# Kernel tuning notes

Hardware: AMD Instinct MI355X
Metric: run time of the kernel (lower is better)

The kernel has to match this reference:

```python
import jax, jax.numpy as jnp
import numpy as np

TOP_K = 2  # num_expert in the torch module


def setup_inputs() -> dict:
    key = jax.random.key(0)
    ks = jax.random.split(key, 8)
    B, C, H, W, E, Dh = 8, 512, 32, 32, 8, 1024
    inputs = jax.random.normal(ks[0], (B, C, H, W), dtype=jnp.float32)
    k = jax.random.uniform(ks[1], (B, 1, 1, 1), dtype=jnp.float32)
    # gate: global-avg-pool + Linear(C -> E)
    Wg = jax.random.normal(ks[2], (C, E), dtype=jnp.float32) / np.sqrt(C)
    bg = jnp.zeros((E,), dtype=jnp.float32)
    # experts: per-expert 2-layer channel MLP (1x1-conv style), modulated by k
    W1 = jax.random.normal(ks[3], (E, C, Dh), dtype=jnp.float32) / np.sqrt(C)
    b1 = jnp.zeros((E, Dh), dtype=jnp.float32)
    W2 = jax.random.normal(ks[4], (E, Dh, C), dtype=jnp.float32) / np.sqrt(Dh)
    b2 = jnp.zeros((E, C), dtype=jnp.float32)
    return {"inputs": inputs, "k": k, "Wg": Wg, "bg": bg,
            "W1": W1, "b1": b1, "W2": W2, "b2": b2}


def reference(inputs, k, Wg, bg, W1, b1, W2, b2):
    B = inputs.shape[0]
    # --- gate: softmax in fp32, cast back (matches F.softmax(dtype=torch.float)) ---
    logits = jnp.mean(inputs, axis=(2, 3)) @ Wg + bg            # [B, E]
    weights = jax.nn.softmax(logits.astype(jnp.float32), axis=1).astype(inputs.dtype)
    topk_w, topk_idx = jax.lax.top_k(weights, TOP_K)            # [B, K]
    # --- scatter top-k gate weights into dense [B, E] mask (training path) ---
    exp_w = jnp.zeros_like(weights).at[jnp.arange(B)[:, None], topk_idx].set(topk_w)
    # --- run ALL experts densely (training-mode math), masked combine ---
    h = jnp.einsum('bchw,ecd->bedhw', inputs, W1) + b1[None, :, :, None, None]
    h = jax.nn.gelu(h, approximate=False)                        # [B,E,Dh,H,W]
    y = jnp.einsum('bedhw,edc->bechw', h, W2) + b2[None, :, :, None, None]
    y = y * k[:, None]                                           # per-sample scalar mod
    out = inputs + jnp.einsum('bechw,be->bchw', y, exp_w)        # residual + weighted sum
    return out
```

## Files before the change

### kernel.cpp

```cpp
#include <hip/hip_runtime.h>
#include <hip/hip_bf16.h>
#include <math.h>


typedef __bf16 bf16_t;
typedef __attribute__((ext_vector_type(8))) __bf16 bf16x8;
typedef __attribute__((ext_vector_type(4))) __bf16 bf16x4;
typedef __attribute__((ext_vector_type(4))) float f32x4;

#define GLDS(g, l) __builtin_amdgcn_global_load_lds(                      \
    (const __attribute__((address_space(1))) void*)(const void*)(g),       \
    (__attribute__((address_space(3))) void*)(void*)(l), 16, 0, 0)

__device__ __forceinline__ float gelu_fast(float x) {
    float z = x * 0.70710678118654752f;
    float az = fabsf(z);
    float t = 1.0f / (1.0f + 0.3275911f * az);
    float p = ((((1.061405429f * t - 1.453152027f) * t + 1.421413741f) * t
                - 0.284496736f) * t + 0.254829592f) * t;
    float e = __expf(-az * az);
    float er = copysignf(1.0f - p * e, z);
    return 0.5f * x * (1.0f + er);
}

__global__ void transpose_cvt_all(const float* __restrict__ x, const float* __restrict__ W1,
                                  const float* __restrict__ W2, bf16_t* __restrict__ xT,
                                  bf16_t* __restrict__ W1t, bf16_t* __restrict__ W2t,
                                  float* __restrict__ msum) {
    int id = blockIdx.x;
    const float* src; bf16_t* dst; int R, Cols, csh; bool dm = false;
    if (id < 4096)      { src = x;  dst = xT;  R = 512;  Cols = 1024; csh = 5; dm = true; }
    else if (id < 8192) { id -= 4096; src = W1; dst = W1t; R = 512;  Cols = 1024; csh = 5; }
    else                { id -= 8192; src = W2; dst = W2t; R = 1024; Cols = 512; csh = 4; }
    const int bz = id >> 9, t = id & 511;
    const int c0 = (t & ((1 << csh) - 1)) * 32, r0 = (t >> csh) * 32;
    const float* s = src + (size_t)bz * R * Cols;
    bf16_t* d = dst + (size_t)bz * R * Cols;
    __shared__ float tile[32][33];
    const int tid = threadIdx.x;
    const int lr = tid >> 3, lc = (tid & 7) * 4;
    float4 v = *(const float4*)(s + (size_t)(r0 + lr) * Cols + c0 + lc);
    tile[lr][lc + 0] = v.x; tile[lr][lc + 1] = v.y;
    tile[lr][lc + 2] = v.z; tile[lr][lc + 3] = v.w;
    if (dm) {
        float ps = v.x + v.y + v.z + v.w;
        ps += __shfl_down(ps, 4, 8);
        ps += __shfl_down(ps, 2, 8);
        ps += __shfl_down(ps, 1, 8);
        if ((tid & 7) == 0) atomicAdd(&msum[bz * 512 + r0 + lr], ps);
    }
    __syncthreads();
    bf16x4 o = { (bf16_t)tile[lc + 0][lr], (bf16_t)tile[lc + 1][lr],
                 (bf16_t)tile[lc + 2][lr], (bf16_t)tile[lc + 3][lr] };
    *(bf16x4*)(d + (size_t)(c0 + lr) * R + r0 + lc) = o;
}

__global__ void gate_kernel(const float* __restrict__ msum, const float* __restrict__ Wg,
                            const float* __restrict__ bg, const float* __restrict__ kmod,
                            int* __restrict__ tidx, float* __restrict__ scale) {
    const int tid = threadIdx.x;
    const int b = tid >> 6, l = tid & 63;
    float a[8] = {0.f, 0.f, 0.f, 0.f, 0.f, 0.f, 0.f, 0.f};
    for (int c = l; c < 512; c += 64) {
        float m = msum[b * 512 + c];
        #pragma unroll
        for (int e = 0; e < 8; ++e) a[e] += m * Wg[c * 8 + e];
    }
    #pragma unroll
    for (int e = 0; e < 8; ++e)
        #pragma unroll
        for (int off = 32; off; off >>= 1) a[e] += __shfl_xor(a[e], off, 64);
    if (l == 0) {
        float lg[8], mx = -1e30f;
        #pragma unroll
        for (int e = 0; e < 8; ++e) { lg[e] = a[e] * (1.0f / 1024.0f) + bg[e]; mx = fmaxf(mx, lg[e]); }
        float sum = 0.f;
        #pragma unroll
        for (int e = 0; e < 8; ++e) { lg[e] = expf(lg[e] - mx); sum += lg[e]; }
        float inv = 1.0f / sum;
        float best = -1.f; int i0 = 0;
        for (int j = 0; j < 8; ++j) { float w = lg[j] * inv; if (w > best) { best = w; i0 = j; } }
        float best2 = -1.f; int i1 = 0;
        for (int j = 0; j < 8; ++j) { if (j == i0) continue; float w = lg[j] * inv; if (w > best2) { best2 = w; i1 = j; } }
        float kb = kmod[b];
        tidx[b * 2] = i0; tidx[b * 2 + 1] = i1;
        scale[b * 2] = best * kb; scale[b * 2 + 1] = best2 * kb;
    }
}

__global__ __launch_bounds__(256, 4) void gemm1_kernel(
    const bf16_t* __restrict__ W1t, const bf16_t* __restrict__ xT,
    const float* __restrict__ b1, const int* __restrict__ tidx,
    const float* __restrict__ scale, bf16_t* __restrict__ hT) {
    __shared__ bf16_t smem[16384];
    const int bid = blockIdx.x;
    const int pair = bid >> 6, rem = bid & 63;
    const int b = pair >> 1, slot = pair & 1;
    const int e = tidx[pair];
    const float s = scale[pair];
    const int d0 = (rem >> 3) * 128, n0 = (rem & 7) * 128;
    const int tid = threadIdx.x;
    const int lane = tid & 63, wave = tid >> 6;
    const int wm = (wave & 1) * 64, wn = (wave >> 1) * 64;
    const int lrow = lane & 15, quad = lane >> 4;

    const bf16_t* gA = W1t + (size_t)e * 524288 + (size_t)d0 * 512;
    const bf16_t* gB = xT + (size_t)b * 524288 + (size_t)n0 * 512;
    const int r0s = tid >> 2, kcs = (tid & 3) * 8;
    f32x4 acc[4][4];
    #pragma unroll
    for (int i = 0; i < 4; ++i)
        #pragma unroll
        for (int j = 0; j < 4; ++j) acc[i][j] = (f32x4){0.f, 0.f, 0.f, 0.f};

    GLDS(gA + r0s * 512 + kcs, smem + tid * 8);
    GLDS(gA + (64 + r0s) * 512 + kcs, smem + (256 + tid) * 8);
    GLDS(gB + r0s * 512 + kcs, smem + 8192 + tid * 8);
    GLDS(gB + (64 + r0s) * 512 + kcs, smem + 8192 + (256 + tid) * 8);
    __syncthreads();

    for (int it = 0; it < 16; ++it) {
        const int cur = it & 1;
        if (it < 15) {
            const int kn = (it + 1) * 32;
            bf16_t* dA = smem + (cur ^ 1) * 4096;
            bf16_t* dB = smem + 8192 + (cur ^ 1) * 4096;
            GLDS(gA + r0s * 512 + kn + kcs, dA + tid * 8);
            GLDS(gA + (64 + r0s) * 512 + kn + kcs, dA + (256 + tid) * 8);
            GLDS(gB + r0s * 512 + kn + kcs, dB + tid * 8);
            GLDS(gB + (64 + r0s) * 512 + kn + kcs, dB + (256 + tid) * 8);
        }
        const bf16_t* cA = smem + cur * 4096;
        const bf16_t* cB = smem + 8192 + cur * 4096;
        bf16x8 af[4], bfr[4];
        #pragma unroll
        for (int i = 0; i < 4; ++i) {
            af[i] = *(const bf16x8*)&cA[(wm + i * 16 + lrow) * 32 + quad * 8];
            bfr[i] = *(const bf16x8*)&cB[(wn + i * 16 + lrow) * 32 + quad * 8];
        }
        #pragma unroll
        for (int i = 0; i < 4; ++i)
            #pragma unroll
            for (int j = 0; j < 4; ++j)
                acc[i][j] = __builtin_amdgcn_mfma_f32_16x16x32_bf16(af[i], bfr[j], acc[i][j], 0, 0, 0);
        __syncthreads();
    }

    bf16_t* hTb = hT + (size_t)b * 2097152 + slot * 1024;
    float4 bb[4];
    #pragma unroll
    for (int i = 0; i < 4; ++i)
        bb[i] = *(const float4*)(b1 + e * 1024 + d0 + wm + i * 16 + quad * 4);

    for (int half = 0; half < 2; ++half) {
        if (wn == half * 64) {
            #pragma unroll
            for (int i = 0; i < 4; ++i)
                #pragma unroll
                for (int j = 0; j < 4; ++j) {
                    const int hw_l = j * 16 + lrow;
                    const int d_l = wm + i * 16 + quad * 4;
                    f32x4 a = acc[i][j];
                    bf16x4 o = { (bf16_t)(gelu_fast(a[0] + bb[i].x) * s),
                                 (bf16_t)(gelu_fast(a[1] + bb[i].y) * s),
                                 (bf16_t)(gelu_fast(a[2] + bb[i].z) * s),
                                 (bf16_t)(gelu_fast(a[3] + bb[i].w) * s) };
                    *(bf16x4*)&smem[hw_l * 136 + d_l] = o;
                }
        }
        __syncthreads();
        #pragma unroll
        for (int q = 0; q < 4; ++q) {
            const int cid = q * 256 + tid;
            const int row = cid >> 4, c16 = cid & 15;
            bf16x8 v = *(const bf16x8*)&smem[row * 136 + c16 * 8];
            *(bf16x8*)(hTb + (size_t)(n0 + half * 64 + row) * 2048 + d0 + c16 * 8) = v;
        }
        __syncthreads();
    }
}

__global__ __launch_bounds__(256, 5) void gemm2_kernel(
    const bf16_t* __restrict__ W2t, const bf16_t* __restrict__ hT,
    const float* __restrict__ b2, const int* __restrict__ tidx,
    const float* __restrict__ scale, const float* __restrict__ x,
    float* __restrict__ out) {
    __shared__ bf16_t smem[16384];
    const int bid = blockIdx.x;
    const int b = bid >> 7, rem = bid & 127;
    const int c0 = (rem >> 4) * 64, n0 = (rem & 15) * 64;
    const int e0 = tidx[b * 2], e1 = tidx[b * 2 + 1];
    const float s0 = scale[b * 2], s1 = scale[b * 2 + 1];
    const int tid = threadIdx.x;
    const int lane = tid & 63, wave = tid >> 6;
    const int wm = (wave & 1) * 32, wn = (wave >> 1) * 32;
    const int lrow = lane & 15, quad = lane >> 4;

    const bf16_t* hTb = hT + (size_t)b * 2097152 + (size_t)n0 * 2048;
    const bf16_t* A0 = W2t + (size_t)e0 * 524288 + (size_t)c0 * 1024;
    const bf16_t* A1 = W2t + (size_t)e1 * 524288 + (size_t)c0 * 1024;
    const int sr = tid >> 2, kcs = (tid & 3) * 8;

    f32x4 acc[2][2];
    #pragma unroll
    for (int i = 0; i < 2; ++i)
        #pragma unroll
        for (int j = 0; j < 2; ++j) acc[i][j] = (f32x4){0.f, 0.f, 0.f, 0.f};

    auto stage = [&](int st, int it) {
        const int k0 = it * 64;
        const bf16_t* gA = ((k0 < 1024) ? A0 : A1) + (size_t)sr * 1024 + (k0 & 1023);
        bf16_t* dA = smem + st * 4096;
        bf16_t* dB = smem + 8192 + st * 4096;
        GLDS(gA + kcs, dA + tid * 8);
        GLDS(gA + 32 + kcs, dA + 2048 + tid * 8);
        const bf16_t* gBp = hTb + (size_t)sr * 2048 + k0;
        GLDS(gBp + kcs, dB + tid * 8);
        GLDS(gBp + 32 + kcs, dB + 2048 + tid * 8);
    };

    stage(0, 0);
    __syncthreads();

    for (int it = 0; it < 32; ++it) {
        const int cur = it & 1;
        if (it < 31) stage(cur ^ 1, it + 1);
        const bf16_t* cA = smem + cur * 4096;
        const bf16_t* cB = smem + 8192 + cur * 4096;
        #pragma unroll
        for (int ks = 0; ks < 2; ++ks) {
            bf16x8 af[2], bfr[2];
            #pragma unroll
            for (int i = 0; i < 2; ++i) {
                af[i] = *(const bf16x8*)&cA[ks * 2048 + (wm + i * 16 + lrow) * 32 + quad * 8];
                bfr[i] = *(const bf16x8*)&cB[ks * 2048 + (wn + i * 16 + lrow) * 32 + quad * 8];
            }
            #pragma unroll
            for (int i = 0; i < 2; ++i)
                #pragma unroll
                for (int j = 0; j < 2; ++j)
                    acc[i][j] = __builtin_amdgcn_mfma_f32_16x16x32_bf16(af[i], bfr[j], acc[i][j], 0, 0, 0);
        }
        __syncthreads();
    }

    #pragma unroll
    for (int i = 0; i < 2; ++i) {
        const int c_l = c0 + wm + i * 16 + quad * 4;
        const float4 bA = *(const float4*)(b2 + e0 * 512 + c_l);
        const float4 bB = *(const float4*)(b2 + e1 * 512 + c_l);
        const float bias[4] = { s0 * bA.x + s1 * bB.x, s0 * bA.y + s1 * bB.y,
                                s0 * bA.z + s1 * bB.z, s0 * bA.w + s1 * bB.w };
        #pragma unroll
        for (int j = 0; j < 2; ++j) {
            const int hw = n0 + wn + j * 16 + lrow;
            #pragma unroll
            for (int r = 0; r < 4; ++r) {
                const size_t o = (size_t)(b * 512 + c_l + r) * 1024 + hw;
                out[o] = x[o] + acc[i][j][r] + bias[r];
            }
        }
    }
}

extern "C" void kernel_launch(void* const* d_in, const int* in_sizes, int n_in,
                              void* d_out, int out_size, void* d_ws, size_t ws_size,
                              hipStream_t stream) {
    const float* x    = (const float*)d_in[0];
    const float* kmod = (const float*)d_in[1];
    const float* Wg   = (const float*)d_in[2];
    const float* bg   = (const float*)d_in[3];
    const float* W1   = (const float*)d_in[4];
    const float* b1   = (const float*)d_in[5];
    const float* W2   = (const float*)d_in[6];
    const float* b2   = (const float*)d_in[7];
    float* out = (float*)d_out;

    char* ws = (char*)d_ws;
    float* msum = (float*)ws;
    float* scl  = (float*)(ws + 16384);
    int*   tix  = (int*)(ws + 16448);
    bf16_t* xT  = (bf16_t*)(ws + 32768);
    bf16_t* W1t = (bf16_t*)(ws + 32768 + (size_t)8388608);
    bf16_t* W2t = (bf16_t*)(ws + 32768 + (size_t)2 * 8388608);
    bf16_t* hT  = (bf16_t*)(ws + 32768 + (size_t)3 * 8388608);

    hipMemsetAsync(msum, 0, 8 * 512 * sizeof(float), stream);
    transpose_cvt_all<<<12288, 256, 0, stream>>>(x, W1, W2, xT, W1t, W2t, msum);
    gate_kernel<<<1, 512, 0, stream>>>(msum, Wg, bg, kmod, tix, scl);
    gemm1_kernel<<<1024, 256, 0, stream>>>(W1t, xT, b1, tix, scl, hT);
    gemm2_kernel<<<1024, 256, 0, stream>>>(W2t, hT, b2, tix, scl, x, out);
}
```

Before: 177.9 us.

## Use 64x64 transpose tiles, drop atomics and memset via partial-sum buffer

```diff
diff --git a/kernel.cpp b/kernel.cpp
--- a/kernel.cpp
+++ b/kernel.cpp
@@ -23,46 +23,61 @@
     return 0.5f * x * (1.0f + er);
 }
 
-__global__ void transpose_cvt_all(const float* __restrict__ x, const float* __restrict__ W1,
-                                  const float* __restrict__ W2, bf16_t* __restrict__ xT,
-                                  bf16_t* __restrict__ W1t, bf16_t* __restrict__ W2t,
-                                  float* __restrict__ msum) {
+__global__ __launch_bounds__(256) void transpose_cvt_all(
+    const float* __restrict__ x, const float* __restrict__ W1,
+    const float* __restrict__ W2, bf16_t* __restrict__ xT,
+    bf16_t* __restrict__ W1t, bf16_t* __restrict__ W2t, float* __restrict__ pp) {
     int id = blockIdx.x;
-    const float* src; bf16_t* dst; int R, Cols, csh; bool dm = false;
-    if (id < 4096)      { src = x;  dst = xT;  R = 512;  Cols = 1024; csh = 5; dm = true; }
-    else if (id < 8192) { id -= 4096; src = W1; dst = W1t; R = 512;  Cols = 1024; csh = 5; }
-    else                { id -= 8192; src = W2; dst = W2t; R = 1024; Cols = 512; csh = 4; }
-    const int bz = id >> 9, t = id & 511;
-    const int c0 = (t & ((1 << csh) - 1)) * 32, r0 = (t >> csh) * 32;
-    const float* s = src + (size_t)bz * R * Cols;
-    bf16_t* d = dst + (size_t)bz * R * Cols;
-    __shared__ float tile[32][33];
+    const float* src; bf16_t* dst; int Rows, Cols, csh; bool dm = false;
+    if (id < 1024)      { src = x;  dst = xT;  Rows = 512;  Cols = 1024; csh = 4; dm = true; }
+    else if (id < 2048) { id -= 1024; src = W1; dst = W1t; Rows = 512;  Cols = 1024; csh = 4; }
+    else                { id -= 2048; src = W2; dst = W2t; Rows = 1024; Cols = 512; csh = 3; }
+    const int bz = id >> 7, t = id & 127;
+    const int ct = t & ((1 << csh) - 1), rt = t >> csh;
+    const int r0 = rt * 64, c0 = ct * 64;
+    __shared__ float tile[64][65];
     const int tid = threadIdx.x;
-    const int lr = tid >> 3, lc = (tid & 7) * 4;
-    float4 v = *(const float4*)(s + (size_t)(r0 + lr) * Cols + c0 + lc);
-    tile[lr][lc + 0] = v.x; tile[lr][lc + 1] = v.y;
-    tile[lr][lc + 2] = v.z; tile[lr][lc + 3] = v.w;
+    const int lrw = tid >> 4, lcol = (tid & 15) * 4;
+    const float* sb = src + (size_t)bz * Rows * Cols + c0;
+    #pragma unroll
+    for (int p = 0; p < 4; ++p) {
+        const int row = p * 16 + lrw;
+        float4 v = *(const float4*)(sb + (size_t)(r0 + row) * Cols + lcol);
+        tile[row][lcol + 0] = v.x; tile[row][lcol + 1] = v.y;
+        tile[row][lcol + 2] = v.z; tile[row][lcol + 3] = v.w;
+    }
+    __syncthreads();
     if (dm) {
-        float ps = v.x + v.y + v.z + v.w;
-        ps += __shfl_down(ps, 4, 8);
-        ps += __shfl_down(ps, 2, 8);
-        ps += __shfl_down(ps, 1, 8);
-        if ((tid & 7) == 0) atomicAdd(&msum[bz * 512 + r0 + lr], ps);
-    }
-    __syncthreads();
-    bf16x4 o = { (bf16_t)tile[lc + 0][lr], (bf16_t)tile[lc + 1][lr],
-                 (bf16_t)tile[lc + 2][lr], (bf16_t)tile[lc + 3][lr] };
-    *(bf16x4*)(d + (size_t)(c0 + lr) * R + r0 + lc) = o;
-}
-
-__global__ void gate_kernel(const float* __restrict__ msum, const float* __restrict__ Wg,
+        const int row = tid >> 2, q = tid & 3;
+        float s = 0.f;
+        #pragma unroll
+        for (int j = 0; j < 16; ++j) s += tile[row][q * 16 + j];
+        s += __shfl_down(s, 2, 4);
+        s += __shfl_down(s, 1, 4);
+        if (q == 0) pp[(bz * 16 + ct) * 512 + r0 + row] = s;
+    }
+    bf16_t* db = dst + (size_t)bz * Rows * Cols + r0;
+    #pragma unroll
+    for (int q = 0; q < 2; ++q) {
+        const int idq = q * 256 + tid;
+        const int orow = idq >> 3, seg = idq & 7;
+        bf16_t ov[8];
+        #pragma unroll
+        for (int j = 0; j < 8; ++j) ov[j] = (bf16_t)tile[seg * 8 + j][orow];
+        *(bf16x8*)(db + (size_t)(c0 + orow) * Rows + seg * 8) = *(bf16x8*)ov;
+    }
+}
+
+__global__ void gate_kernel(const float* __restrict__ pp, const float* __restrict__ Wg,
                             const float* __restrict__ bg, const float* __restrict__ kmod,
                             int* __restrict__ tidx, float* __restrict__ scale) {
     const int tid = threadIdx.x;
     const int b = tid >> 6, l = tid & 63;
     float a[8] = {0.f, 0.f, 0.f, 0.f, 0.f, 0.f, 0.f, 0.f};
     for (int c = l; c < 512; c += 64) {
-        float m = msum[b * 512 + c];
+        float m = 0.f;
+        #pragma unroll
+        for (int ht = 0; ht < 16; ++ht) m += pp[(b * 16 + ht) * 512 + c];
         #pragma unroll
         for (int e = 0; e < 8; ++e) a[e] += m * Wg[c * 8 + e];
     }
@@ -107,6 +122,7 @@
     const bf16_t* gA = W1t + (size_t)e * 524288 + (size_t)d0 * 512;
     const bf16_t* gB = xT + (size_t)b * 524288 + (size_t)n0 * 512;
     const int r0s = tid >> 2, kcs = (tid & 3) * 8;
+
     f32x4 acc[4][4];
     #pragma unroll
     for (int i = 0; i < 4; ++i)
@@ -152,6 +168,7 @@
     for (int i = 0; i < 4; ++i)
         bb[i] = *(const float4*)(b1 + e * 1024 + d0 + wm + i * 16 + quad * 4);
 
+    #pragma unroll
     for (int half = 0; half < 2; ++half) {
         if (wn == half * 64) {
             #pragma unroll
@@ -277,17 +294,16 @@
     float* out = (float*)d_out;
 
     char* ws = (char*)d_ws;
-    float* msum = (float*)ws;
-    float* scl  = (float*)(ws + 16384);
-    int*   tix  = (int*)(ws + 16448);
+    int*   tix  = (int*)ws;
+    float* scl  = (float*)(ws + 64);
     bf16_t* xT  = (bf16_t*)(ws + 32768);
     bf16_t* W1t = (bf16_t*)(ws + 32768 + (size_t)8388608);
     bf16_t* W2t = (bf16_t*)(ws + 32768 + (size_t)2 * 8388608);
     bf16_t* hT  = (bf16_t*)(ws + 32768 + (size_t)3 * 8388608);
-
-    hipMemsetAsync(msum, 0, 8 * 512 * sizeof(float), stream);
-    transpose_cvt_all<<<12288, 256, 0, stream>>>(x, W1, W2, xT, W1t, W2t, msum);
-    gate_kernel<<<1, 512, 0, stream>>>(msum, Wg, bg, kmod, tix, scl);
+    float* pp   = (float*)hT;
+
+    transpose_cvt_all<<<3072, 256, 0, stream>>>(x, W1, W2, xT, W1t, W2t, pp);
+    gate_kernel<<<1, 512, 0, stream>>>(pp, Wg, bg, kmod, tix, scl);
     gemm1_kernel<<<1024, 256, 0, stream>>>(W1t, xT, b1, tix, scl, hT);
     gemm2_kernel<<<1024, 256, 0, stream>>>(W2t, hT, b2, tix, scl, x, out);
 }
```

Result: no change. 179.8 us (+1.1%).
